# Performance work log

Measured on AMD Instinct MI355X. Metric: run time of the kernel, lower is better.

## Reference

```python
import jax, jax.numpy as jnp
import numpy as np

N_NODES = 50000
N_EDGES = 600000
D = 128
LAYERS = 2


def setup_inputs() -> dict:
    key = jax.random.key(0)
    ks = jax.random.split(key, 7)
    row = jax.random.randint(ks[0], (N_EDGES,), 0, N_NODES, dtype=jnp.int32)
    col = jax.random.randint(ks[1], (N_EDGES,), 0, N_NODES, dtype=jnp.int32)
    vals = jax.random.normal(ks[2], (N_EDGES,), dtype=jnp.float32)
    X = jax.random.normal(ks[3], (N_NODES, D), dtype=jnp.float32)
    temps = jax.random.normal(ks[4], (LAYERS, D), dtype=jnp.float32) * 0.1
    W = jax.random.normal(ks[5], (LAYERS, D, D), dtype=jnp.float32) * (1.0 / np.sqrt(D))
    b = jax.random.normal(ks[6], (LAYERS, D), dtype=jnp.float32) * 0.01
    return {"row": row, "col": col, "vals": vals, "X": X, "temps": temps, "W": W, "b": b}


def reference(row, col, vals, X, temps, W, b):
    # Iterated: X <- relu(Linear_i(X - temp_i * (Lap @ X)))
    for i in range(LAYERS):
        # spmm via COO edge list: LX[r] = sum_e vals[e] * X[col[e]] for edges with row[e]==r
        msgs = vals[:, None] * X[col]            # [E, D] gather + scale
        LX = jax.ops.segment_sum(msgs, row, num_segments=N_NODES)  # [N, D] scatter-add
        X = X - temps[i] * LX                    # elementwise scale-subtract
        X = jax.nn.relu(X @ W[i].T + b[i])       # Linear (torch: x W^T + b) + ReLU
    return X
```

## Files before the change

### kernel.cpp

```cpp
#include <hip/hip_runtime.h>

#define N_NODES 50000
#define N_EDGES 600000
#define D 128
#define LAYERS 2
#define NAL 50048
#define CAP 48
#define NB1 256
#define EPB 2344
#define NBINS 256
#define BIN_ROWS 196
#define FRAG_CAP 32
#define PBLOCKS 6250

typedef short bf16x8 __attribute__((ext_vector_type(8)));
typedef float f32x4 __attribute__((ext_vector_type(4)));
typedef float f32x2 __attribute__((ext_vector_type(2)));

__device__ __forceinline__ ushort f2b(float f) {
  uint u = __float_as_uint(f);
  return (ushort)((u + 0x7fffu + ((u >> 16) & 1u)) >> 16);
}
__device__ __forceinline__ float b2f_lo(uint p) { return __uint_as_float(p << 16); }
__device__ __forceinline__ float b2f_hi(uint p) { return __uint_as_float(p & 0xffff0000u); }

__global__ __launch_bounds__(256) void k_bin_prep(
    const int* __restrict__ row, const int* __restrict__ col,
    const float* __restrict__ vals,
    uint2* __restrict__ staging, int* __restrict__ bcnt,
    const float* __restrict__ X, const float* __restrict__ W,
    ushort* __restrict__ Xb, ushort* __restrict__ Wb, uint* __restrict__ Xf8) {
  const int blk = blockIdx.x;
  const int t = threadIdx.x;
  if (blk < NB1) {
    __shared__ int lcur[NBINS];
    lcur[t] = 0;
    __syncthreads();
    const int e0 = blk * EPB;
    for (int i = t; i < EPB; i += 256) {
      int e = e0 + i;
      if (e < N_EDGES) {
        int r = row[e];
        int bin = r / BIN_ROWS;
        int slot = atomicAdd(&lcur[bin], 1);
        if (slot < FRAG_CAP) {
          uint cv = ((uint)f2b(vals[e]) << 16) | (uint)col[e];
          staging[((size_t)blk * NBINS + bin) * FRAG_CAP + slot] =
              make_uint2(cv, (uint)r);
        }
      }
    }
    __syncthreads();
    bcnt[blk * NBINS + t] = min(lcur[t], FRAG_CAP);
  } else {
    int i = (blk - NB1) * 256 + t;
    if (i < N_NODES * D / 4) {
      float4 v = ((const float4*)X)[i];
      ushort4 o;
      o.x = f2b(v.x); o.y = f2b(v.y); o.z = f2b(v.z); o.w = f2b(v.w);
      ((ushort4*)Xb)[i] = o;
      int pk = __builtin_amdgcn_cvt_pk_fp8_f32(v.x, v.y, 0, false);
      pk = __builtin_amdgcn_cvt_pk_fp8_f32(v.z, v.w, pk, true);
      Xf8[i] = (uint)pk;
    }
    if (i < LAYERS * D * D / 4) {
      float4 v = ((const float4*)W)[i];
      ushort4 o;
      o.x = f2b(v.x); o.y = f2b(v.y); o.z = f2b(v.z); o.w = f2b(v.w);
      ((ushort4*)Wb)[i] = o;
    }
  }
}

__global__ __launch_bounds__(256) void k_scatter(
    const uint2* __restrict__ staging, const int* __restrict__ bcnt,
    int* __restrict__ counts, uint* __restrict__ ell) {
  const int b = blockIdx.x;
  const int t = threadIdx.x;
  __shared__ int lcur[BIN_ROWS];
  for (int i = t; i < BIN_ROWS; i += 256) lcur[i] = 0;
  __syncthreads();
  const int rbase = b * BIN_ROWS;
  const int n = bcnt[t * NBINS + b];
  const uint2* frag = staging + ((size_t)t * NBINS + b) * FRAG_CAP;
  for (int k = 0; k < n; ++k) {
    uint2 E = frag[k];
    int rl = (int)E.y - rbase;
    int slot = atomicAdd(&lcur[rl], 1);
    if (slot < CAP) ell[(size_t)E.y * CAP + slot] = E.x;
  }
  __syncthreads();
  for (int i = t; i < BIN_ROWS; i += 256) {
    int r = rbase + i;
    if (r < NAL) counts[r] = lcur[i];
  }
}

__global__ __launch_bounds__(256) void k_layer(
    const int* __restrict__ counts, const uint* __restrict__ ell,
    const ushort* __restrict__ Xin, const uchar* __restrict__ Xg8,
    const ushort* __restrict__ Wb, const float* __restrict__ bias,
    const float* __restrict__ temps_l,
    ushort* __restrict__ Yb, uchar* __restrict__ Yf8,
    float* __restrict__ Yf, int store_f32) {
  __shared__ ushort Xs[16][136];
  const int t = threadIdx.x;

  {
    const int nloc = t >> 4;
    const int c = t & 15;
    const int g = blockIdx.x * 16 + nloc;
    const uint* ep = ell + (size_t)g * CAP;
    int cnt = counts[g];
    if (cnt > CAP) cnt = CAP;
    float a0 = 0.f, a1 = 0.f, a2 = 0.f, a3 = 0.f;
    float a4 = 0.f, a5 = 0.f, a6 = 0.f, a7 = 0.f;
#define EDGE_FMA(v, q)                                                  \
    {                                                                   \
      f32x2 f0 = __builtin_amdgcn_cvt_pk_f32_fp8((q).x, false);         \
      f32x2 f1 = __builtin_amdgcn_cvt_pk_f32_fp8((q).x, true);          \
      f32x2 f2 = __builtin_amdgcn_cvt_pk_f32_fp8((q).y, false);         \
      f32x2 f3 = __builtin_amdgcn_cvt_pk_f32_fp8((q).y, true);          \
      a0 = fmaf(v, f0.x, a0); a1 = fmaf(v, f0.y, a1);                   \
      a2 = fmaf(v, f1.x, a2); a3 = fmaf(v, f1.y, a3);                   \
      a4 = fmaf(v, f2.x, a4); a5 = fmaf(v, f2.y, a5);                   \
      a6 = fmaf(v, f3.x, a6); a7 = fmaf(v, f3.y, a7);                   \
    }
    uint4 eb = *(const uint4*)ep;
    int j = 0;
    for (; j + 4 <= cnt; j += 4) {
      uint4 en = *(const uint4*)(ep + j + 4);
      uint2 q0 = *(const uint2*)(Xg8 + ((size_t)(eb.x & 0xFFFFu) << 7) + c * 8);
      uint2 q1 = *(const uint2*)(Xg8 + ((size_t)(eb.y & 0xFFFFu) << 7) + c * 8);
      uint2 q2 = *(const uint2*)(Xg8 + ((size_t)(eb.z & 0xFFFFu) << 7) + c * 8);
      uint2 q3 = *(const uint2*)(Xg8 + ((size_t)(eb.w & 0xFFFFu) << 7) + c * 8);
      float v0 = b2f_hi(eb.x), v1 = b2f_hi(eb.y);
      float v2 = b2f_hi(eb.z), v3 = b2f_hi(eb.w);
      EDGE_FMA(v0, q0); EDGE_FMA(v1, q1); EDGE_FMA(v2, q2); EDGE_FMA(v3, q3);
      eb = en;
    }
    for (; j < cnt; ++j) {
      uint e = ep[j];
      uint2 q = *(const uint2*)(Xg8 + ((size_t)(e & 0xFFFFu) << 7) + c * 8);
      float v = b2f_hi(e);
      EDGE_FMA(v, q);
    }
#undef EDGE_FMA
    uint4 pr = *(const uint4*)(Xin + ((size_t)g << 7) + c * 8);
    float4 t0 = *(const float4*)(temps_l + c * 8);
    float4 t1 = *(const float4*)(temps_l + c * 8 + 4);
    uint r0 = (uint)f2b(b2f_lo(pr.x) - t0.x * a0) | ((uint)f2b(b2f_hi(pr.x) - t0.y * a1) << 16);
    uint r1 = (uint)f2b(b2f_lo(pr.y) - t0.z * a2) | ((uint)f2b(b2f_hi(pr.y) - t0.w * a3) << 16);
    uint r2 = (uint)f2b(b2f_lo(pr.z) - t1.x * a4) | ((uint)f2b(b2f_hi(pr.z) - t1.y * a5) << 16);
    uint r3 = (uint)f2b(b2f_lo(pr.w) - t1.z * a6) | ((uint)f2b(b2f_hi(pr.w) - t1.w * a7) << 16);
    *(uint4*)&Xs[nloc][c * 8] = make_uint4(r0, r1, r2, r3);
  }
  __syncthreads();

  const int wave = t >> 6;
  const int lane = t & 63;
  const int lr = lane & 15;
  const int kg = lane >> 4;

  bf16x8 a0 = *(const bf16x8*)&Xs[lr][0 + kg * 8];
  bf16x8 a1 = *(const bf16x8*)&Xs[lr][32 + kg * 8];
  bf16x8 a2 = *(const bf16x8*)&Xs[lr][64 + kg * 8];
  bf16x8 a3 = *(const bf16x8*)&Xs[lr][96 + kg * 8];

  const int crow = kg * 4;
  #pragma unroll
  for (int q = 0; q < 2; ++q) {
    const int nt = wave * 2 + q;
    const ushort* wp = Wb + ((size_t)(nt * 16 + lr) << 7) + kg * 8;
    bf16x8 b0 = *(const bf16x8*)(wp);
    bf16x8 b1 = *(const bf16x8*)(wp + 32);
    bf16x8 b2 = *(const bf16x8*)(wp + 64);
    bf16x8 b3 = *(const bf16x8*)(wp + 96);
    f32x4 acc = {0.f, 0.f, 0.f, 0.f};
    acc = __builtin_amdgcn_mfma_f32_16x16x32_bf16(a0, b0, acc, 0, 0, 0);
    acc = __builtin_amdgcn_mfma_f32_16x16x32_bf16(a1, b1, acc, 0, 0, 0);
    acc = __builtin_amdgcn_mfma_f32_16x16x32_bf16(a2, b2, acc, 0, 0, 0);
    acc = __builtin_amdgcn_mfma_f32_16x16x32_bf16(a3, b3, acc, 0, 0, 0);
    const int col = nt * 16 + lr;
    const float bv = bias[col];
    if (store_f32) {
      #pragma unroll
      for (int r = 0; r < 4; ++r) {
        int grow = blockIdx.x * 16 + crow + r;
        if (grow < N_NODES)
          Yf[((size_t)grow << 7) + col] = fmaxf(acc[r] + bv, 0.f);
      }
    } else {
      #pragma unroll
      for (int r = 0; r < 4; ++r) {
        int grow = blockIdx.x * 16 + crow + r;
        float o = fmaxf(acc[r] + bv, 0.f);
        Yb[((size_t)grow << 7) + col] = f2b(o);
        int pk = __builtin_amdgcn_cvt_pk_fp8_f32(o, o, 0, false);
        Yf8[((size_t)grow << 7) + col] = (uchar)(pk & 0xff);
      }
    }
  }
}

extern "C" void kernel_launch(void* const* d_in, const int* in_sizes, int n_in,
                              void* d_out, int out_size, void* d_ws, size_t ws_size,
                              hipStream_t stream) {
  const int*   row   = (const int*)d_in[0];
  const int*   col   = (const int*)d_in[1];
  const float* vals  = (const float*)d_in[2];
  const float* X     = (const float*)d_in[3];
  const float* temps = (const float*)d_in[4];
  const float* W     = (const float*)d_in[5];
  const float* b     = (const float*)d_in[6];
  float* Y = (float*)d_out;

  int*    counts  = (int*)d_ws;
  int*    bcnt    = counts + NAL;
  uint2*  staging = (uint2*)(bcnt + NB1 * NBINS);
  uint*   ell     = (uint*)(staging + (size_t)NB1 * NBINS * FRAG_CAP);
  ushort* Xb      = (ushort*)(ell + (size_t)NAL * CAP);
  ushort* Yb      = Xb + (size_t)NAL * D;
  ushort* Wb      = Yb + (size_t)NAL * D;
  uchar*  Xf8     = (uchar*)(Wb + LAYERS * D * D);
  uchar*  Yf8     = Xf8 + (size_t)NAL * D;

  const int lblocks = NAL / 16;

  k_bin_prep<<<NB1 + PBLOCKS, 256, 0, stream>>>(row, col, vals, staging, bcnt,
                                                X, W, Xb, Wb, (uint*)Xf8);
  k_scatter<<<NBINS, 256, 0, stream>>>(staging, bcnt, counts, ell);

  k_layer<<<lblocks, 256, 0, stream>>>(counts, ell, Xb, Xf8, Wb, b, temps,
                                       Yb, Yf8, nullptr, 0);
  k_layer<<<lblocks, 256, 0, stream>>>(counts, ell, Yb, Yf8, Wb + D * D, b + D,
                                       temps + D, nullptr, nullptr, Y, 1);
}
```

Measured before the change: 91.26 us.

## Split fp8 gather into column-half passes to shrink per-pass working set

Stores the fp8 feature copy as two separate 64-column planes and splits each layer's SpMM into two kernels. Each kernel gathers only one half, so the random-access working set per pass is halved, which is meant to fit better in cache. The first half's result goes through a bf16 intermediate buffer that the second kernel reads back before the MFMA linear step. Each block now covers 32 rows, and the gather loop is unrolled to 8 edges. This adds kernel launches and traffic for the intermediate, and the edge list is read twice per layer.

```diff
diff --git a/kernel.cpp b/kernel.cpp
--- a/kernel.cpp
+++ b/kernel.cpp
@@ -16,6 +16,7 @@
 typedef short bf16x8 __attribute__((ext_vector_type(8)));
 typedef float f32x4 __attribute__((ext_vector_type(4)));
 typedef float f32x2 __attribute__((ext_vector_type(2)));
+typedef uint  u32x4 __attribute__((ext_vector_type(4)));
 
 __device__ __forceinline__ ushort f2b(float f) {
   uint u = __float_as_uint(f);
@@ -29,7 +30,8 @@
     const float* __restrict__ vals,
     uint2* __restrict__ staging, int* __restrict__ bcnt,
     const float* __restrict__ X, const float* __restrict__ W,
-    ushort* __restrict__ Xb, ushort* __restrict__ Wb, uint* __restrict__ Xf8) {
+    ushort* __restrict__ Xb, ushort* __restrict__ Wb,
+    uint* __restrict__ X8a, uint* __restrict__ X8b) {
   const int blk = blockIdx.x;
   const int t = threadIdx.x;
   if (blk < NB1) {
@@ -61,7 +63,9 @@
       ((ushort4*)Xb)[i] = o;
       int pk = __builtin_amdgcn_cvt_pk_fp8_f32(v.x, v.y, 0, false);
       pk = __builtin_amdgcn_cvt_pk_fp8_f32(v.z, v.w, pk, true);
-      Xf8[i] = (uint)pk;
+      int r = i >> 5, cg = i & 31;
+      if (cg < 16) X8a[r * 16 + cg] = (uint)pk;
+      else         X8b[r * 16 + cg - 16] = (uint)pk;
     }
     if (i < LAYERS * D * D / 4) {
       float4 v = ((const float4*)W)[i];
@@ -96,25 +100,47 @@
   }
 }
 
-__global__ __launch_bounds__(256) void k_layer(
-    const int* __restrict__ counts, const uint* __restrict__ ell,
-    const ushort* __restrict__ Xin, const uchar* __restrict__ Xg8,
-    const ushort* __restrict__ Wb, const float* __restrict__ bias,
-    const float* __restrict__ temps_l,
-    ushort* __restrict__ Yb, uchar* __restrict__ Yf8,
-    float* __restrict__ Yf, int store_f32) {
-  __shared__ ushort Xs[16][136];
-  const int t = threadIdx.x;
-
-  {
-    const int nloc = t >> 4;
-    const int c = t & 15;
-    const int g = blockIdx.x * 16 + nloc;
-    const uint* ep = ell + (size_t)g * CAP;
-    int cnt = counts[g];
-    if (cnt > CAP) cnt = CAP;
-    float a0 = 0.f, a1 = 0.f, a2 = 0.f, a3 = 0.f;
-    float a4 = 0.f, a5 = 0.f, a6 = 0.f, a7 = 0.f;
+#define GATHER_HALF(X8)                                                      \
+    float a0 = 0.f, a1 = 0.f, a2 = 0.f, a3 = 0.f;                            \
+    float a4 = 0.f, a5 = 0.f, a6 = 0.f, a7 = 0.f;                            \
+    {                                                                        \
+      uint4 ea = *(const uint4*)(ep);                                        \
+      uint4 eb = *(const uint4*)(ep + 4);                                    \
+      int j = 0;                                                             \
+      for (; j + 8 <= cnt; j += 8) {                                         \
+        uint4 na = *(const uint4*)(ep + j + 8);                              \
+        uint4 nb = *(const uint4*)(ep + j + 12);                             \
+        uint2 q0 = *(const uint2*)((X8) + ((size_t)(ea.x & 0xFFFFu) << 6) + c * 8); \
+        uint2 q1 = *(const uint2*)((X8) + ((size_t)(ea.y & 0xFFFFu) << 6) + c * 8); \
+        uint2 q2 = *(const uint2*)((X8) + ((size_t)(ea.z & 0xFFFFu) << 6) + c * 8); \
+        uint2 q3 = *(const uint2*)((X8) + ((size_t)(ea.w & 0xFFFFu) << 6) + c * 8); \
+        uint2 q4 = *(const uint2*)((X8) + ((size_t)(eb.x & 0xFFFFu) << 6) + c * 8); \
+        uint2 q5 = *(const uint2*)((X8) + ((size_t)(eb.y & 0xFFFFu) << 6) + c * 8); \
+        uint2 q6 = *(const uint2*)((X8) + ((size_t)(eb.z & 0xFFFFu) << 6) + c * 8); \
+        uint2 q7 = *(const uint2*)((X8) + ((size_t)(eb.w & 0xFFFFu) << 6) + c * 8); \
+        EDGE_FMA(b2f_hi(ea.x), q0); EDGE_FMA(b2f_hi(ea.y), q1);              \
+        EDGE_FMA(b2f_hi(ea.z), q2); EDGE_FMA(b2f_hi(ea.w), q3);              \
+        EDGE_FMA(b2f_hi(eb.x), q4); EDGE_FMA(b2f_hi(eb.y), q5);              \
+        EDGE_FMA(b2f_hi(eb.z), q6); EDGE_FMA(b2f_hi(eb.w), q7);              \
+        ea = na; eb = nb;                                                    \
+      }                                                                      \
+      if (j + 4 <= cnt) {                                                    \
+        uint2 q0 = *(const uint2*)((X8) + ((size_t)(ea.x & 0xFFFFu) << 6) + c * 8); \
+        uint2 q1 = *(const uint2*)((X8) + ((size_t)(ea.y & 0xFFFFu) << 6) + c * 8); \
+        uint2 q2 = *(const uint2*)((X8) + ((size_t)(ea.z & 0xFFFFu) << 6) + c * 8); \
+        uint2 q3 = *(const uint2*)((X8) + ((size_t)(ea.w & 0xFFFFu) << 6) + c * 8); \
+        EDGE_FMA(b2f_hi(ea.x), q0); EDGE_FMA(b2f_hi(ea.y), q1);              \
+        EDGE_FMA(b2f_hi(ea.z), q2); EDGE_FMA(b2f_hi(ea.w), q3);              \
+        ea = eb;                                                             \
+        j += 4;                                                              \
+      }                                                                      \
+      for (; j < cnt; ++j) {                                                 \
+        uint e = ep[j];                                                      \
+        uint2 q = *(const uint2*)((X8) + ((size_t)(e & 0xFFFFu) << 6) + c * 8); \
+        EDGE_FMA(b2f_hi(e), q);                                              \
+      }                                                                      \
+    }
+
 #define EDGE_FMA(v, q)                                                  \
     {                                                                   \
       f32x2 f0 = __builtin_amdgcn_cvt_pk_f32_fp8((q).x, false);         \
@@ -126,34 +152,62 @@
       a4 = fmaf(v, f2.x, a4); a5 = fmaf(v, f2.y, a5);                   \
       a6 = fmaf(v, f3.x, a6); a7 = fmaf(v, f3.y, a7);                   \
     }
-    uint4 eb = *(const uint4*)ep;
-    int j = 0;
-    for (; j + 4 <= cnt; j += 4) {
-      uint4 en = *(const uint4*)(ep + j + 4);
-      uint2 q0 = *(const uint2*)(Xg8 + ((size_t)(eb.x & 0xFFFFu) << 7) + c * 8);
-      uint2 q1 = *(const uint2*)(Xg8 + ((size_t)(eb.y & 0xFFFFu) << 7) + c * 8);
-      uint2 q2 = *(const uint2*)(Xg8 + ((size_t)(eb.z & 0xFFFFu) << 7) + c * 8);
-      uint2 q3 = *(const uint2*)(Xg8 + ((size_t)(eb.w & 0xFFFFu) << 7) + c * 8);
-      float v0 = b2f_hi(eb.x), v1 = b2f_hi(eb.y);
-      float v2 = b2f_hi(eb.z), v3 = b2f_hi(eb.w);
-      EDGE_FMA(v0, q0); EDGE_FMA(v1, q1); EDGE_FMA(v2, q2); EDGE_FMA(v3, q3);
-      eb = en;
-    }
-    for (; j < cnt; ++j) {
-      uint e = ep[j];
-      uint2 q = *(const uint2*)(Xg8 + ((size_t)(e & 0xFFFFu) << 7) + c * 8);
-      float v = b2f_hi(e);
-      EDGE_FMA(v, q);
-    }
-#undef EDGE_FMA
-    uint4 pr = *(const uint4*)(Xin + ((size_t)g << 7) + c * 8);
-    float4 t0 = *(const float4*)(temps_l + c * 8);
-    float4 t1 = *(const float4*)(temps_l + c * 8 + 4);
-    uint r0 = (uint)f2b(b2f_lo(pr.x) - t0.x * a0) | ((uint)f2b(b2f_hi(pr.x) - t0.y * a1) << 16);
-    uint r1 = (uint)f2b(b2f_lo(pr.y) - t0.z * a2) | ((uint)f2b(b2f_hi(pr.y) - t0.w * a3) << 16);
-    uint r2 = (uint)f2b(b2f_lo(pr.z) - t1.x * a4) | ((uint)f2b(b2f_hi(pr.z) - t1.y * a5) << 16);
-    uint r3 = (uint)f2b(b2f_lo(pr.w) - t1.z * a6) | ((uint)f2b(b2f_hi(pr.w) - t1.w * a7) << 16);
-    *(uint4*)&Xs[nloc][c * 8] = make_uint4(r0, r1, r2, r3);
+
+__global__ __launch_bounds__(256) void k_lo(
+    const int* __restrict__ counts, const uint* __restrict__ ell,
+    const ushort* __restrict__ Xdiag, const uchar* __restrict__ X8,
+    const float* __restrict__ temps_l, ushort* __restrict__ P1) {
+  const int t = threadIdx.x;
+  const int nloc = t >> 3;
+  const int c = t & 7;
+  const int g = blockIdx.x * 32 + nloc;
+  const uint* ep = ell + (size_t)g * CAP;
+  int cnt = counts[g];
+  if (cnt > CAP) cnt = CAP;
+  GATHER_HALF(X8)
+  u32x4 pr = __builtin_nontemporal_load(
+      (const u32x4*)(Xdiag + ((size_t)g << 7) + c * 8));
+  float4 t0 = *(const float4*)(temps_l + c * 8);
+  float4 t1 = *(const float4*)(temps_l + c * 8 + 4);
+  u32x4 outv;
+  outv.x = (uint)f2b(b2f_lo(pr.x) - t0.x * a0) | ((uint)f2b(b2f_hi(pr.x) - t0.y * a1) << 16);
+  outv.y = (uint)f2b(b2f_lo(pr.y) - t0.z * a2) | ((uint)f2b(b2f_hi(pr.y) - t0.w * a3) << 16);
+  outv.z = (uint)f2b(b2f_lo(pr.z) - t1.x * a4) | ((uint)f2b(b2f_hi(pr.z) - t1.y * a5) << 16);
+  outv.w = (uint)f2b(b2f_lo(pr.w) - t1.z * a6) | ((uint)f2b(b2f_hi(pr.w) - t1.w * a7) << 16);
+  __builtin_nontemporal_store(outv, (u32x4*)(P1 + (size_t)g * 64 + c * 8));
+}
+
+__global__ __launch_bounds__(256) void k_hi(
+    const int* __restrict__ counts, const uint* __restrict__ ell,
+    const ushort* __restrict__ Xdiag, const uchar* __restrict__ X8,
+    const ushort* __restrict__ Wb, const float* __restrict__ bias,
+    const float* __restrict__ temps_l, const ushort* __restrict__ P1,
+    ushort* __restrict__ Yb, uchar* __restrict__ Y8a, uchar* __restrict__ Y8b,
+    float* __restrict__ Yf, int store_f32) {
+  __shared__ ushort Xs[32][136];
+  const int t = threadIdx.x;
+
+  {
+    const int nloc = t >> 3;
+    const int c = t & 7;
+    const int g = blockIdx.x * 32 + nloc;
+    const uint* ep = ell + (size_t)g * CAP;
+    int cnt = counts[g];
+    if (cnt > CAP) cnt = CAP;
+    GATHER_HALF(X8)
+    u32x4 pr = __builtin_nontemporal_load(
+        (const u32x4*)(Xdiag + ((size_t)g << 7) + 64 + c * 8));
+    float4 t0 = *(const float4*)(temps_l + 64 + c * 8);
+    float4 t1 = *(const float4*)(temps_l + 64 + c * 8 + 4);
+    u32x4 hv;
+    hv.x = (uint)f2b(b2f_lo(pr.x) - t0.x * a0) | ((uint)f2b(b2f_hi(pr.x) - t0.y * a1) << 16);
+    hv.y = (uint)f2b(b2f_lo(pr.y) - t0.z * a2) | ((uint)f2b(b2f_hi(pr.y) - t0.w * a3) << 16);
+    hv.z = (uint)f2b(b2f_lo(pr.z) - t1.x * a4) | ((uint)f2b(b2f_hi(pr.z) - t1.y * a5) << 16);
+    hv.w = (uint)f2b(b2f_lo(pr.w) - t1.z * a6) | ((uint)f2b(b2f_hi(pr.w) - t1.w * a7) << 16);
+    *(u32x4*)&Xs[nloc][64 + c * 8] = hv;
+    u32x4 p1v = __builtin_nontemporal_load(
+        (const u32x4*)(P1 + (size_t)g * 64 + c * 8));
+    *(u32x4*)&Xs[nloc][c * 8] = p1v;
   }
   __syncthreads();
 
@@ -161,16 +215,17 @@
   const int lane = t & 63;
   const int lr = lane & 15;
   const int kg = lane >> 4;
-
-  bf16x8 a0 = *(const bf16x8*)&Xs[lr][0 + kg * 8];
-  bf16x8 a1 = *(const bf16x8*)&Xs[lr][32 + kg * 8];
-  bf16x8 a2 = *(const bf16x8*)&Xs[lr][64 + kg * 8];
-  bf16x8 a3 = *(const bf16x8*)&Xs[lr][96 + kg * 8];
+  const int rt = (wave >> 1) * 16;
+
+  bf16x8 a0 = *(const bf16x8*)&Xs[rt + lr][0 + kg * 8];
+  bf16x8 a1 = *(const bf16x8*)&Xs[rt + lr][32 + kg * 8];
+  bf16x8 a2 = *(const bf16x8*)&Xs[rt + lr][64 + kg * 8];
+  bf16x8 a3 = *(const bf16x8*)&Xs[rt + lr][96 + kg * 8];
 
   const int crow = kg * 4;
   #pragma unroll
-  for (int q = 0; q < 2; ++q) {
-    const int nt = wave * 2 + q;
+  for (int q = 0; q < 4; ++q) {
+    const int nt = (wave & 1) * 4 + q;
     const ushort* wp = Wb + ((size_t)(nt * 16 + lr) << 7) + kg * 8;
     bf16x8 b0 = *(const bf16x8*)(wp);
     bf16x8 b1 = *(const bf16x8*)(wp + 32);
@@ -186,18 +241,20 @@
     if (store_f32) {
       #pragma unroll
       for (int r = 0; r < 4; ++r) {
-        int grow = blockIdx.x * 16 + crow + r;
+        int grow = blockIdx.x * 32 + rt + crow + r;
         if (grow < N_NODES)
           Yf[((size_t)grow << 7) + col] = fmaxf(acc[r] + bv, 0.f);
       }
     } else {
       #pragma unroll
       for (int r = 0; r < 4; ++r) {
-        int grow = blockIdx.x * 16 + crow + r;
+        int grow = blockIdx.x * 32 + rt + crow + r;
         float o = fmaxf(acc[r] + bv, 0.f);
         Yb[((size_t)grow << 7) + col] = f2b(o);
         int pk = __builtin_amdgcn_cvt_pk_fp8_f32(o, o, 0, false);
-        Yf8[((size_t)grow << 7) + col] = (uchar)(pk & 0xff);
+        uchar byte = (uchar)(pk & 0xff);
+        if (col < 64) Y8a[(size_t)grow * 64 + col] = byte;
+        else          Y8b[(size_t)grow * 64 + col - 64] = byte;
       }
     }
   }
@@ -222,17 +279,24 @@
   ushort* Xb      = (ushort*)(ell + (size_t)NAL * CAP);
   ushort* Yb      = Xb + (size_t)NAL * D;
   ushort* Wb      = Yb + (size_t)NAL * D;
-  uchar*  Xf8     = (uchar*)(Wb + LAYERS * D * D);
-  uchar*  Yf8     = Xf8 + (size_t)NAL * D;
-
-  const int lblocks = NAL / 16;
+  ushort* P1      = Wb + LAYERS * D * D;
+  uchar*  X8a     = (uchar*)(P1 + (size_t)NAL * 64);
+  uchar*  X8b     = X8a + (size_t)NAL * 64;
+  uchar*  Y8a     = X8b + (size_t)NAL * 64;
+  uchar*  Y8b     = Y8a + (size_t)NAL * 64;
+
+  const int hblocks = NAL / 32;
 
   k_bin_prep<<<NB1 + PBLOCKS, 256, 0, stream>>>(row, col, vals, staging, bcnt,
-                                                X, W, Xb, Wb, (uint*)Xf8);
+                                                X, W, Xb, Wb,
+                                                (uint*)X8a, (uint*)X8b);
   k_scatter<<<NBINS, 256, 0, stream>>>(staging, bcnt, counts, ell);
 
-  k_layer<<<lblocks, 256, 0, stream>>>(counts, ell, Xb, Xf8, Wb, b, temps,
-                                       Yb, Yf8, nullptr, 0);
-  k_layer<<<lblocks, 256, 0, stream>>>(counts, ell, Yb, Yf8, Wb + D * D, b + D,
-                                       temps + D, nullptr, nullptr, Y, 1);
-}
+  k_lo<<<hblocks, 256, 0, stream>>>(counts, ell, Xb, X8a, temps, P1);
+  k_hi<<<hblocks, 256, 0, stream>>>(counts, ell, Xb, X8b, Wb, b, temps, P1,
+                                    Yb, Y8a, Y8b, nullptr, 0);
+  k_lo<<<hblocks, 256, 0, stream>>>(counts, ell, Yb, Y8a, temps + D, P1);
+  k_hi<<<hblocks, 256, 0, stream>>>(counts, ell, Yb, Y8b, Wb + D * D, b + D,
+                                    temps + D, P1, nullptr, nullptr, nullptr,
+                                    Y, 1);
+}
```

Measured after the change: 104.2 us. 1.14x slower.
